# Optimization experiments

Measured on AMD Instinct MI355X. Metric: run time of the kernel, lower is better.

The kernel has to match this reference:

```python
import jax, jax.numpy as jnp
import numpy as np
import math

B, S, HID, H, DH = 4, 1024, 1024, 16, 64  # batch, seq, hidden, heads, head_dim


def _rotate_half(x):
    x1, x2 = jnp.split(x, 2, axis=-1)
    return jnp.concatenate([-x2, x1], axis=-1)


def _apply_rope(t, freqs):
    # t: [B,H,S,DH], freqs: [S,rot_dim]; here rot_dim == DH so no pass-through part
    rot = freqs.shape[-1]
    cos_ = jnp.cos(freqs)[None, None, :, :].astype(t.dtype)
    sin_ = jnp.sin(freqs)[None, None, :, :].astype(t.dtype)
    t_rot, t_pass = t[..., :rot], t[..., rot:]
    t_rot = t_rot * cos_ + _rotate_half(t_rot) * sin_
    return jnp.concatenate([t_rot, t_pass], axis=-1)


def setup_inputs() -> dict:
    key = jax.random.key(0)
    ks = jax.random.split(key, 8)
    hidden_states = jax.random.normal(ks[0], (B, S, HID), dtype=jnp.float32)
    # additive mask: valid prefix of random length per batch row, -1e9 on padding
    lengths = jax.random.randint(ks[1], (B,), 3 * S // 4, S + 1)
    pos = jnp.arange(S)
    attention_mask = jnp.where(pos[None, :] < lengths[:, None], 0.0, -1e9)
    attention_mask = attention_mask.astype(jnp.float32)[:, None, None, :]  # [B,1,1,S]
    # rotary frequencies: standard RoPE angles, duplicated halves -> [S, DH]
    inv_freq = 1.0 / (10000.0 ** (jnp.arange(0, DH // 2, dtype=jnp.float32) / (DH // 2)))
    ang = pos.astype(jnp.float32)[:, None] * inv_freq[None, :]
    freqs = jnp.concatenate([ang, ang], axis=-1)  # [S, DH]
    sc = 0.02
    Wq = jax.random.normal(ks[2], (HID, HID), dtype=jnp.float32) * sc
    Wk = jax.random.normal(ks[3], (HID, HID), dtype=jnp.float32) * sc
    Wv = jax.random.normal(ks[4], (HID, HID), dtype=jnp.float32) * sc
    bq = jnp.zeros((HID,), dtype=jnp.float32)
    bk = jnp.zeros((HID,), dtype=jnp.float32)
    bv = jnp.zeros((HID,), dtype=jnp.float32)
    return dict(hidden_states=hidden_states, attention_mask=attention_mask, freqs=freqs,
                Wq=Wq, bq=bq, Wk=Wk, bk=bk, Wv=Wv, bv=bv)


def reference(hidden_states, attention_mask, freqs, Wq, bq, Wk, bk, Wv, bv):
    b, s, _ = hidden_states.shape
    # QKV projections -> [B,H,S,DH]
    q = (hidden_states @ Wq + bq).reshape(b, s, H, DH).transpose(0, 2, 1, 3)
    k = (hidden_states @ Wk + bk).reshape(b, s, H, DH).transpose(0, 2, 1, 3)
    v = (hidden_states @ Wv + bv).reshape(b, s, H, DH).transpose(0, 2, 1, 3)
    # inline RoPE on q and k (same freqs for both, as (rotary_pos_emb,)*2)
    q = _apply_rope(q, freqs)
    k = _apply_rope(k, freqs)
    scores = jnp.einsum('bhqd,bhkd->bhqk', q, k) / math.sqrt(DH)
    scores = scores + attention_mask  # additive mask broadcast over [B,H,S,S]
    probs = jax.nn.softmax(scores, axis=-1)
    # no_prob_mask filtering: zero out masked key columns
    probs = jnp.where(attention_mask < -1e-5, 0.0, probs)
    # dropout prob is 0.0 (eval) -> identity
    ctx = jnp.einsum('bhqk,bhkd->bhqd', probs, v)
    ctx = ctx.transpose(0, 2, 1, 3).reshape(b, s, H * DH)
    return ctx
```

## Files before the change

kernel.cpp:

```cpp
#include <hip/hip_runtime.h>
#include <hip/hip_bf16.h>
#include <cmath>

#define NB   4
#define NS   1024
#define NHID 1024
#define NH   16
#define NDH  64
#define QKV_PLANE (NB * NH * NS * NDH)

typedef __attribute__((ext_vector_type(8))) short bf16x8;
typedef __attribute__((ext_vector_type(4))) float f32x4;
typedef __attribute__((ext_vector_type(8))) unsigned short u16x8;

typedef __attribute__((address_space(1))) const void gv_t;
typedef __attribute__((address_space(3))) void       lv_t;

__device__ __forceinline__ void gload16(const void* g, void* l) {
    __builtin_amdgcn_global_load_lds((gv_t*)g, (lv_t*)l, 16, 0, 0);
}

__device__ __forceinline__ unsigned short f2b(float f) {
    union { float f; unsigned int u; } v; v.f = f;
    unsigned int r = (v.u + 0x7fff + ((v.u >> 16) & 1)) >> 16;
    return (unsigned short)r;
}

__device__ __forceinline__ unsigned int f2b2(float a, float b) {
    __hip_bfloat162 h = __float22bfloat162_rn(make_float2(a, b));
    union { __hip_bfloat162 h; unsigned int u; } v; v.h = h;
    return v.u;
}

__device__ __forceinline__ float fexp2(float x) {
#if __has_builtin(__builtin_amdgcn_exp2f)
    return __builtin_amdgcn_exp2f(x);
#else
    return exp2f(x);
#endif
}

#define VMWAIT(N) do { \
    asm volatile("s_waitcnt vmcnt(" #N ")" ::: "memory"); \
    __builtin_amdgcn_sched_barrier(0); } while (0)

#define SBAR() do { \
    __builtin_amdgcn_sched_barrier(0); \
    __builtin_amdgcn_s_barrier(); \
    __builtin_amdgcn_sched_barrier(0); } while (0)

__global__ __launch_bounds__(256) void prep_kernel(
    const float* __restrict__ hs, const float* __restrict__ freqs,
    const float* __restrict__ Wq, const float* __restrict__ Wk,
    const float* __restrict__ Wv,
    unsigned short* __restrict__ hsb, unsigned short* __restrict__ wt,
    float2* __restrict__ cs)
{
    const int z   = blockIdx.z;
    const int tid = threadIdx.x;

    if (z == 3) {
        const int bx = blockIdx.y * 16 + blockIdx.x;
        #pragma unroll
        for (int c = 0; c < 16; ++c) {
            const int idx = bx * 16384 + (c * 256 + tid) * 4;
            float4 v = *(const float4*)&hs[idx];
            ushort4 o;
            o.x = f2b(v.x); o.y = f2b(v.y); o.z = f2b(v.z); o.w = f2b(v.w);
            *(ushort4*)&hsb[idx] = o;
        }
        return;
    }
    if (z == 4) {
        const int bx = blockIdx.y * 16 + blockIdx.x;
        if (bx < 128) {
            const int id = bx * 256 + tid;
            const int s = id >> 5, d = id & 31;
            const float ang = freqs[s * NDH + d];
            float sn, cn;
            sincosf(ang, &sn, &cn);
            cs[id] = make_float2(cn, sn);
        }
        return;
    }

    const float* __restrict__ W = (z == 0) ? Wq : (z == 1) ? Wk : Wv;
    __shared__ float t[64][65];
    const int k0 = blockIdx.x * 64, n0 = blockIdx.y * 64;
    #pragma unroll
    for (int c = 0; c < 16; ++c) {
        const int flat = c * 256 + tid;
        const int r = flat >> 6, cc = flat & 63;
        t[r][cc] = W[(size_t)(k0 + r) * NHID + n0 + cc];
    }
    __syncthreads();
    #pragma unroll
    for (int c = 0; c < 16; ++c) {
        const int flat = c * 256 + tid;
        const int r = flat >> 6, cc = flat & 63;
        wt[(size_t)(z * 1024 + n0 + r) * NHID + k0 + cc] = f2b(t[cc][r]);
    }
}

__global__ __launch_bounds__(256) void fused_gemm_kernel(
    const unsigned short* __restrict__ hsb,
    const unsigned short* __restrict__ wt,
    const float2* __restrict__ cs,
    const float* __restrict__ bq, const float* __restrict__ bk,
    const float* __restrict__ bv,
    unsigned short* __restrict__ qkv)
{
    __shared__ short SH[24576];

    const int tid  = threadIdx.x;
    const int lane = tid & 63;
    const int wv   = __builtin_amdgcn_readfirstlane(tid >> 6);

    const int hw  = blockIdx.x + 24 * blockIdx.y;
    const int xcd = hw & 7;
    const int j   = hw >> 3;
    const int tx  = (xcd & 1) * 12 + (j % 12);
    const int ty  = (xcd >> 1) * 8 + (j / 12);

    const bool vmode = (tx >= 16);

    const unsigned short* Amat;
    const unsigned short* Bmat;
    int a_base, b_base, m0, n0, vb_ = 0;
    if (!vmode) {
        n0 = tx * 128;
        m0 = ty * 128;
        Amat = hsb;  a_base = m0;
        Bmat = wt;   b_base = n0;
    } else {
        m0  = (tx - 16) * 128;
        vb_ = ty >> 3;
        n0  = (ty & 7) * 128;
        Amat = wt;   a_base = 2048 + m0;
        Bmat = hsb;  b_base = vb_ * 1024 + n0;
    }

    const int srow = lane >> 2;
    const int skc  = ((lane & 3) ^ ((lane >> 3) & 3)) * 8;
    const unsigned short* gA1 = Amat + (size_t)(a_base + 16 * wv + srow) * NHID + skc;
    const unsigned short* gA2 = gA1 + (size_t)64 * NHID;
    const unsigned short* gB1 = Bmat + (size_t)(b_base + 16 * wv + srow) * NHID + skc;
    const unsigned short* gB2 = gB1 + (size_t)64 * NHID;

#define STAGE(S, T) do { \
    short* Sb_ = SH + (S) * 8192 + 512 * wv; \
    const size_t ko_ = (size_t)(T) * 32; \
    gload16(gA1 + ko_, Sb_); \
    gload16(gA2 + ko_, Sb_ + 2048); \
    gload16(gB1 + ko_, Sb_ + 4096); \
    gload16(gB2 + ko_, Sb_ + 6144); \
} while (0)

    const int R  = (wv & 1) * 64;
    const int CW = (wv >> 1) * 64;
    const int c0 = lane & 15;
    const int g  = lane >> 4;
    const int swz  = (g ^ ((c0 >> 1) & 3)) * 8;
    const int aofl = (R + c0) * 32 + swz;
    const int bofl = 4096 + (CW + c0) * 32 + swz;

    f32x4 acc[4][4] = {};

#define COMP(S) do { \
    const short* Sc_ = SH + (S) * 8192; \
    bf16x8 af[4], bfr[4]; \
    _Pragma("unroll") \
    for (int i_ = 0; i_ < 4; ++i_) af[i_]  = *(const bf16x8*)&Sc_[aofl + 512 * i_]; \
    _Pragma("unroll") \
    for (int j_ = 0; j_ < 4; ++j_) bfr[j_] = *(const bf16x8*)&Sc_[bofl + 512 * j_]; \
    __builtin_amdgcn_s_setprio(1); \
    _Pragma("unroll") \
    for (int i_ = 0; i_ < 4; ++i_) \
        _Pragma("unroll") \
        for (int j_ = 0; j_ < 4; ++j_) \
            acc[i_][j_] = __builtin_amdgcn_mfma_f32_16x16x32_bf16( \
                af[i_], bfr[j_], acc[i_][j_], 0, 0, 0); \
    __builtin_amdgcn_s_setprio(0); \
} while (0)

    STAGE(0, 0);
    STAGE(1, 1);
    VMWAIT(4);
    SBAR();

    #pragma unroll 1
    for (int tb = 0; tb < 30; tb += 3) {
        STAGE(2, tb + 2); COMP(0); VMWAIT(4); SBAR();
        STAGE(0, tb + 3); COMP(1); VMWAIT(4); SBAR();
        STAGE(1, tb + 4); COMP(2); VMWAIT(4); SBAR();
    }
    COMP(0); VMWAIT(0); SBAR();
    COMP(1);
#undef STAGE
#undef COMP

    __syncthreads();
    unsigned short* E = (unsigned short*)SH;
    const int qrow4 = g * 4;

    if (!vmode) {
        const int z  = n0 >> 10;
        const int hd = ((n0 & 1023) + CW) >> 6;
        const float* __restrict__ bb = (z == 0) ? bq : bk;
        const float b0 = bb[hd * 64 + c0];
        const float b1 = bb[hd * 64 + c0 + 16];
        const float b2 = bb[hd * 64 + c0 + 32];
        const float b3 = bb[hd * 64 + c0 + 48];

        #pragma unroll
        for (int i = 0; i < 4; ++i) {
            #pragma unroll
            for (int r = 0; r < 4; ++r) {
                const int ml = R + qrow4 + 16 * i + r;
                const int s  = (m0 + ml) & 1023;
                float o0 = acc[i][0][r] + b0;
                float o1 = acc[i][1][r] + b1;
                float o2 = acc[i][2][r] + b2;
                float o3 = acc[i][3][r] + b3;
                const float2 cs0 = cs[s * 32 + c0];
                const float2 cs1 = cs[s * 32 + c0 + 16];
                unsigned short* e = E + ml * 132 + CW + c0;
                e[0]  = f2b(o0 * cs0.x - o2 * cs0.y);
                e[16] = f2b(o1 * cs1.x - o3 * cs1.y);
                e[32] = f2b(o2 * cs0.x + o0 * cs0.y);
                e[48] = f2b(o3 * cs1.x + o1 * cs1.y);
            }
        }
        __syncthreads();

        const int hd0 = (n0 & 1023) >> 6;
        unsigned short* __restrict__ base = qkv + (size_t)z * QKV_PLANE;
        #pragma unroll
        for (int c = 0; c < 8; ++c) {
            const int chunk = c * 256 + tid;
            const int row   = chunk >> 4;
            const int col16 = chunk & 15;
            const int m     = m0 + row;
            const int bidx  = m >> 10;
            const int s     = m & 1023;
            const int head  = hd0 + (col16 >> 3);
            const int d     = (col16 & 7) * 8;
            u16x8 v = *(const u16x8*)&E[row * 132 + col16 * 8];
            *(u16x8*)&base[(((size_t)bidx * NH + head) * NS + s) * NDH + d] = v;
        }
    } else {
        #pragma unroll
        for (int i = 0; i < 4; ++i) {
            #pragma unroll
            for (int r = 0; r < 4; ++r) {
                const int ml  = R + qrow4 + 16 * i + r;
                const float bvm = bv[m0 + ml];
                unsigned short* e = E + ml * 132 + CW + c0;
                e[0]  = f2b(acc[i][0][r] + bvm);
                e[16] = f2b(acc[i][1][r] + bvm);
                e[32] = f2b(acc[i][2][r] + bvm);
                e[48] = f2b(acc[i][3][r] + bvm);
            }
        }
        __syncthreads();

        unsigned short* __restrict__ vplane = qkv + 2 * (size_t)QKV_PLANE;
        #pragma unroll
        for (int c = 0; c < 8; ++c) {
            const int chunk = c * 256 + tid;
            const int row   = chunk >> 4;
            const int col16 = chunk & 15;
            u16x8 v = *(const u16x8*)&E[row * 132 + col16 * 8];
            *(u16x8*)&vplane[((size_t)(vb_ * 1024 + m0 + row)) * NS
                             + n0 + col16 * 8] = v;
        }
    }
}

__global__ __launch_bounds__(512) void attn_kernel(
    const unsigned short* __restrict__ qkv, const float* __restrict__ mask,
    float* __restrict__ out)
{
    const int hw  = blockIdx.x + 8 * (blockIdx.y + 16 * blockIdx.z);
    const int xcd = hw & 7;
    const int j   = hw >> 3;
    const int hb  = xcd * 8 + (j & 7);
    const int qt  = j >> 3;
    const int h   = hb & 15, b = hb >> 4;

    const unsigned short* qp  = qkv + ((size_t)(b * NH + h) * NS) * NDH;
    const unsigned short* kp  = qp + QKV_PLANE;
    const unsigned short* vtp = qkv + 2 * (size_t)QKV_PLANE
                              + ((size_t)(b * NH + h) * NDH) * NS;

    __shared__ unsigned short KsA[3][64 * 64];
    __shared__ unsigned short VtA[3][64 * 64];
    __shared__ unsigned short PsA[128 * 64];
    __shared__ float Ll[128];

    const int tid  = threadIdx.x;
    const int lane = tid & 63;
    const int w    = __builtin_amdgcn_readfirstlane(tid >> 6);
    const int c0   = lane & 15;
    const int g    = lane >> 4;
    const int sw7  = c0 & 7;
    const float C1 = 0.125f * 1.44269504f;
    const float L2E = 1.44269504f;
    const float* __restrict__ mrow = mask + (size_t)b * NS;

    float mval = -2.0f;
    if (lane < 16) mval = mrow[lane * 64];

    bf16x8 qf[2];
    #pragma unroll
    for (int ks = 0; ks < 2; ++ks)
        qf[ks] = *(const bf16x8*)&qp[
            (size_t)(qt * 128 + w * 16 + c0) * NDH + g * 8 + ks * 32];

    const int i8 = lane >> 3, c8 = lane & 7;
    const int gsw = (c8 ^ i8) * 8;
    const unsigned short* gk0 = kp  + (size_t)(w * 8 + i8) * NDH + gsw;
    const unsigned short* gv0 = vtp + (size_t)(w * 8 + i8) * NS  + gsw;

    int kaddr[4][2], pw4[4], pr[2];
    #pragma unroll
    for (int mt = 0; mt < 4; ++mt)
        #pragma unroll
        for (int ks = 0; ks < 2; ++ks)
            kaddr[mt][ks] = (mt * 16 + c0) * 64 + ((g + ks * 4) ^ sw7) * 8;
    #pragma unroll
    for (int mt = 0; mt < 4; ++mt)
        pw4[mt] = (w * 16 + c0) * 64 + ((2 * mt + (g >> 1)) ^ sw7) * 8 + (g & 1) * 4;
    #pragma unroll
    for (int ks = 0; ks < 2; ++ks)
        pr[ks] = (w * 16 + c0) * 64 + ((g + ks * 4) ^ sw7) * 8;

    gload16(gk0,                &KsA[0][w * 512]);
    gload16(gv0,                &VtA[0][w * 512]);
    gload16(gk0 + 64 * NDH,     &KsA[1][w * 512]);
    gload16(gv0 + 64,           &VtA[1][w * 512]);

    int ktmax = __popcll(__ballot(mval >= -1.0f));
    if (ktmax < 1) ktmax = 1;

    VMWAIT(2);
    SBAR();

    float lrow = 0.f;
    f32x4 O[4] = {};

    int sl = 0;
    for (int kt = 0; kt < ktmax; ++kt) {
        const bool more1 = (kt + 1 < ktmax);
        const bool more2 = (kt + 2 < ktmax);

        float4 mkf[4];
        #pragma unroll
        for (int mt = 0; mt < 4; ++mt)
            mkf[mt] = *(const float4*)&mrow[kt * 64 + mt * 16 + g * 4];
        __builtin_amdgcn_sched_barrier(0);

        if (more2) {
            const int s2 = (sl >= 1) ? sl - 1 : sl + 2;
            gload16(gk0 + (size_t)(kt + 2) * 64 * NDH, &KsA[s2][w * 512]);
            gload16(gv0 + (size_t)(kt + 2) * 64,       &VtA[s2][w * 512]);
        }

        const unsigned short* Kb = KsA[sl];
        const unsigned short* Vb = VtA[sl];

        bf16x8 kf[4][2];
        #pragma unroll
        for (int mt = 0; mt < 4; ++mt)
            #pragma unroll
            for (int ks = 0; ks < 2; ++ks)
                kf[mt][ks] = *(const bf16x8*)&Kb[kaddr[mt][ks]];
        f32x4 S[4];
        __builtin_amdgcn_s_setprio(1);
        #pragma unroll
        for (int mt = 0; mt < 4; ++mt) {
            f32x4 a = {};
            a = __builtin_amdgcn_mfma_f32_16x16x32_bf16(kf[mt][0], qf[0], a, 0, 0, 0);
            a = __builtin_amdgcn_mfma_f32_16x16x32_bf16(kf[mt][1], qf[1], a, 0, 0, 0);
            S[mt] = a;
        }
        __builtin_amdgcn_s_setprio(0);

        float psum = 0.f;
        #pragma unroll
        for (int mt = 0; mt < 4; ++mt) {
            float p0 = fexp2(S[mt][0] * C1 + mkf[mt].x * L2E);
            float p1 = fexp2(S[mt][1] * C1 + mkf[mt].y * L2E);
            float p2 = fexp2(S[mt][2] * C1 + mkf[mt].z * L2E);
            float p3 = fexp2(S[mt][3] * C1 + mkf[mt].w * L2E);
            psum += (p0 + p1) + (p2 + p3);
            uint2 u;
            u.x = f2b2(p0, p1);
            u.y = f2b2(p2, p3);
            *(uint2*)&PsA[pw4[mt]] = u;
        }
        lrow += psum;

        bf16x8 pf[2], vf[4][2];
        #pragma unroll
        for (int ks = 0; ks < 2; ++ks)
            pf[ks] = *(const bf16x8*)&PsA[pr[ks]];
        #pragma unroll
        for (int nd = 0; nd < 4; ++nd)
            #pragma unroll
            for (int ks = 0; ks < 2; ++ks)
                vf[nd][ks] = *(const bf16x8*)&Vb[kaddr[nd][ks]];
        __builtin_amdgcn_s_setprio(1);
        #pragma unroll
        for (int nd = 0; nd < 4; ++nd) {
            f32x4 o = O[nd];
            o = __builtin_amdgcn_mfma_f32_16x16x32_bf16(pf[0], vf[nd][0], o, 0, 0, 0);
            o = __builtin_amdgcn_mfma_f32_16x16x32_bf16(pf[1], vf[nd][1], o, 0, 0, 0);
            O[nd] = o;
        }
        __builtin_amdgcn_s_setprio(0);

        if (more1) {
            if (more2) { VMWAIT(2); }
            else       { VMWAIT(0); }
            SBAR();
        }
        sl = (sl == 2) ? 0 : sl + 1;
    }

    lrow += __shfl_xor(lrow, 16);
    lrow += __shfl_xor(lrow, 32);
    if (g == 0) Ll[w * 16 + c0] = lrow;
    float4 lv4 = *(const float4*)&Ll[w * 16 + g * 4];
    float inv[4];
    #pragma unroll
    for (int r = 0; r < 4; ++r) inv[r] = 1.0f / ((const float*)&lv4)[r];

    #pragma unroll
    for (int nd = 0; nd < 4; ++nd)
        #pragma unroll
        for (int r = 0; r < 4; ++r) {
            const int row = qt * 128 + w * 16 + g * 4 + r;
            const int col = h * 64 + nd * 16 + c0;
            out[((size_t)b * NS + row) * NHID + col] = O[nd][r] * inv[r];
        }
}

extern "C" void kernel_launch(void* const* d_in, const int* in_sizes, int n_in,
                              void* d_out, int out_size, void* d_ws, size_t ws_size,
                              hipStream_t stream) {
    const float* hs    = (const float*)d_in[0];
    const float* mask  = (const float*)d_in[1];
    const float* freqs = (const float*)d_in[2];
    const float* Wq    = (const float*)d_in[3];
    const float* bq    = (const float*)d_in[4];
    const float* Wk    = (const float*)d_in[5];
    const float* bk    = (const float*)d_in[6];
    const float* Wv    = (const float*)d_in[7];
    const float* bv    = (const float*)d_in[8];
    float* out = (float*)d_out;

    char* ws = (char*)d_ws;
    unsigned short* qkvb = (unsigned short*)ws;
    unsigned short* hsb  = (unsigned short*)(ws + 25165824);
    unsigned short* wtb  = (unsigned short*)(ws + 33554432);
    float2*         csb  = (float2*)       (ws + 39845888);

    prep_kernel<<<dim3(16, 16, 5), 256, 0, stream>>>(hs, freqs, Wq, Wk, Wv,
                                                     hsb, wtb, csb);
    fused_gemm_kernel<<<dim3(24, 32), 256, 0, stream>>>(hsb, wtb, csb,
                                                        bq, bk, bv, qkvb);
    attn_kernel<<<dim3(NS / 128, NH, NB), 512, 0, stream>>>(qkvb, mask, out);
}
```

Measured before the change: 151.7 us.

## Feed softmax probabilities to PV MFMA from registers via 16x16x16 bf16

Removes the LDS round-trip for the probability tile by packing the exp values directly into bf16x4 register operands and using the 16x16x16 bf16 MFMA, which consumes the S accumulator layout as its A operand. This drops the PsA shared buffer, its stores and reloads, and lowers LDS usage. In exchange the PV product issues twice as many smaller MFMAs with 8-byte V reads instead of 16-byte reads, which may lower MFMA throughput.

```diff
diff --git a/kernel.cpp b/kernel.cpp
--- a/kernel.cpp
+++ b/kernel.cpp
@@ -10,8 +10,15 @@
 #define QKV_PLANE (NB * NH * NS * NDH)
 
 typedef __attribute__((ext_vector_type(8))) short bf16x8;
+typedef __attribute__((ext_vector_type(4))) short bf16x4;
 typedef __attribute__((ext_vector_type(4))) float f32x4;
 typedef __attribute__((ext_vector_type(8))) unsigned short u16x8;
+
+#if __has_builtin(__builtin_amdgcn_mfma_f32_16x16x16bf16_1k)
+#define MFMA16 1
+#else
+#define MFMA16 0
+#endif
 
 typedef __attribute__((address_space(1))) const void gv_t;
 typedef __attribute__((address_space(3))) void       lv_t;
@@ -295,7 +302,9 @@
 
     __shared__ unsigned short KsA[3][64 * 64];
     __shared__ unsigned short VtA[3][64 * 64];
+#if !MFMA16
     __shared__ unsigned short PsA[128 * 64];
+#endif
     __shared__ float Ll[128];
 
     const int tid  = threadIdx.x;
@@ -322,18 +331,27 @@
     const unsigned short* gk0 = kp  + (size_t)(w * 8 + i8) * NDH + gsw;
     const unsigned short* gv0 = vtp + (size_t)(w * 8 + i8) * NS  + gsw;
 
-    int kaddr[4][2], pw4[4], pr[2];
+    int kaddr[4][2];
     #pragma unroll
     for (int mt = 0; mt < 4; ++mt)
         #pragma unroll
         for (int ks = 0; ks < 2; ++ks)
             kaddr[mt][ks] = (mt * 16 + c0) * 64 + ((g + ks * 4) ^ sw7) * 8;
+#if MFMA16
+    int vk[4];
+    #pragma unroll
+    for (int mt = 0; mt < 4; ++mt)
+        vk[mt] = ((2 * mt + (g >> 1)) ^ sw7) * 8 + (g & 1) * 4;
+    const int vrow = c0 * 64;
+#else
+    int pw4[4], pr[2];
     #pragma unroll
     for (int mt = 0; mt < 4; ++mt)
         pw4[mt] = (w * 16 + c0) * 64 + ((2 * mt + (g >> 1)) ^ sw7) * 8 + (g & 1) * 4;
     #pragma unroll
     for (int ks = 0; ks < 2; ++ks)
         pr[ks] = (w * 16 + c0) * 64 + ((g + ks * 4) ^ sw7) * 8;
+#endif
 
     gload16(gk0,                &KsA[0][w * 512]);
     gload16(gv0,                &VtA[0][w * 512]);
@@ -387,6 +405,9 @@
         __builtin_amdgcn_s_setprio(0);
 
         float psum = 0.f;
+#if MFMA16
+        bf16x4 pa[4];
+#endif
         #pragma unroll
         for (int mt = 0; mt < 4; ++mt) {
             float p0 = fexp2(S[mt][0] * C1 + mkf[mt].x * L2E);
@@ -394,13 +415,31 @@
             float p2 = fexp2(S[mt][2] * C1 + mkf[mt].z * L2E);
             float p3 = fexp2(S[mt][3] * C1 + mkf[mt].w * L2E);
             psum += (p0 + p1) + (p2 + p3);
-            uint2 u;
-            u.x = f2b2(p0, p1);
-            u.y = f2b2(p2, p3);
-            *(uint2*)&PsA[pw4[mt]] = u;
+            union { uint2 u; bf16x4 v; } cv;
+            cv.u.x = f2b2(p0, p1);
+            cv.u.y = f2b2(p2, p3);
+#if MFMA16
+            pa[mt] = cv.v;
+#else
+            *(uint2*)&PsA[pw4[mt]] = cv.u;
+#endif
         }
         lrow += psum;
 
+#if MFMA16
+        __builtin_amdgcn_s_setprio(1);
+        #pragma unroll
+        for (int nd = 0; nd < 4; ++nd) {
+            f32x4 o = O[nd];
+            #pragma unroll
+            for (int mt = 0; mt < 4; ++mt) {
+                bf16x4 vb = *(const bf16x4*)&Vb[vrow + nd * 1024 + vk[mt]];
+                o = __builtin_amdgcn_mfma_f32_16x16x16bf16_1k(pa[mt], vb, o, 0, 0, 0);
+            }
+            O[nd] = o;
+        }
+        __builtin_amdgcn_s_setprio(0);
+#else
         bf16x8 pf[2], vf[4][2];
         #pragma unroll
         for (int ks = 0; ks < 2; ++ks)
@@ -419,6 +458,7 @@
             O[nd] = o;
         }
         __builtin_amdgcn_s_setprio(0);
+#endif
 
         if (more1) {
             if (more2) { VMWAIT(2); }
```

Result: no change. 153.4 us (+1.1%).
